# Performance work log

Hardware: AMD Instinct MI355X
Metric: run time of the kernel (lower is better)

The kernel has to match this reference:

```python
import jax, jax.numpy as jnp
import numpy as np

HEADS = 4
DIM_HEAD = 32


def setup_inputs() -> dict:
    key = jax.random.key(0)
    k0, k1, k2, k3 = jax.random.split(key, 4)
    b, C, H, W = 32, 128, 64, 64
    hidden = HEADS * DIM_HEAD
    x = jax.random.normal(k0, (b, C, H, W), dtype=jnp.float32)
    g = jnp.ones((C,), dtype=jnp.float32)                      # RMSNorm gain
    w_qkv = jax.random.normal(k1, (3 * hidden, C), dtype=jnp.float32) * 0.05
    mem_kv = jax.random.normal(k2, (2, HEADS, DIM_HEAD, 4), dtype=jnp.float32)
    w_out = jax.random.normal(k3, (C, hidden), dtype=jnp.float32) * 0.05
    b_out = jnp.zeros((C,), dtype=jnp.float32)
    return {"x": x, "g": g, "w_qkv": w_qkv, "mem_kv": mem_kv,
            "w_out": w_out, "b_out": b_out}


def reference(x, g, w_qkv, mem_kv, w_out, b_out):
    b, C, H, W = x.shape
    heads = mem_kv.shape[1]
    dh = mem_kv.shape[2]
    hidden = heads * dh
    scale = dh ** -0.5

    # RMSNorm variant: F.normalize along channel dim * g * sqrt(C)
    norm = jnp.maximum(jnp.sqrt(jnp.sum(x * x, axis=1, keepdims=True)), 1e-12)
    xn = x / norm * g[None, :, None, None] * (C ** 0.5)

    # 1x1 conv qkv projection (no bias)
    qkv = jnp.einsum('bchw,oc->bohw', xn, w_qkv)  # [b, 3*hidden, H, W]
    q, k, v = jnp.split(qkv, 3, axis=1)
    n = H * W
    q = q.reshape(b, heads, dh, n)
    k = k.reshape(b, heads, dh, n)
    v = v.reshape(b, heads, dh, n)

    # prepend memory kv slots along the token dim
    mk = jnp.broadcast_to(mem_kv[0][None], (b, heads, dh, mem_kv.shape[3]))
    mv = jnp.broadcast_to(mem_kv[1][None], (b, heads, dh, mem_kv.shape[3]))
    k = jnp.concatenate([mk, k], axis=-1)
    v = jnp.concatenate([mv, v], axis=-1)

    q = jax.nn.softmax(q, axis=-2) * scale   # softmax over feature dim d
    k = jax.nn.softmax(k, axis=-1)           # softmax over token dim n

    context = jnp.einsum('bhdn,bhen->bhde', k, v)   # [b,h,d,e]
    out = jnp.einsum('bhde,bhdn->bhen', context, q)  # [b,h,e,n]
    out = out.reshape(b, hidden, H, W)

    # 1x1 conv output projection (with bias)
    return jnp.einsum('bchw,oc->bohw', out, w_out) + b_out[None, :, None, None]
```

## Files before the change

kernel.cpp:

```cpp
#include <hip/hip_runtime.h>
#include <hip/hip_bf16.h>

typedef __attribute__((ext_vector_type(8))) short short8;
typedef __attribute__((ext_vector_type(4))) float f32x4;


__device__ __forceinline__ unsigned short f2bf(float f) {
  unsigned u = __float_as_uint(f);
  u += 0x7fff + ((u >> 16) & 1);
  return (unsigned short)(u >> 16);
}

__global__ void k0_init(const float* __restrict__ wqkv, const float* __restrict__ g,
                        float* __restrict__ ws) {
  int tid = blockIdx.x * blockDim.x + threadIdx.x;
  int stride = gridDim.x * blockDim.x;
  unsigned short* Wf = (unsigned short*)(ws + 2424832);
  for (int i = tid; i < 49152; i += stride) {
    int o = i >> 7, c = i & 127;
    int f = (o >> 4) * 4 + (c >> 5);
    int lane = (o & 15) + (((c >> 3) & 3) << 4);
    Wf[f * 512 + lane * 8 + (c & 7)] = f2bf(wqkv[o * 128 + c]);
  }
  float* gs = ws + 2449408;
  if (tid < 128) gs[tid] = g[tid] * 11.313708498984761f;
}

__global__ __launch_bounds__(256) void k1_qkv(
    const float* __restrict__ x, const unsigned short* __restrict__ Wf,
    const float* __restrict__ gs, float* __restrict__ Sp, float* __restrict__ Zp,
    unsigned short* __restrict__ qbf) {
  __shared__ __align__(16) unsigned short xnf[16 * 512];
  __shared__ unsigned short kbuf[128 * 66];
  __shared__ unsigned short vbuf[128 * 66];
  __shared__ float ssred[256];
  const int b = blockIdx.x >> 4, grp = blockIdx.x & 15;
  const int tid = threadIdx.x;
  const int p = tid & 63, w = tid >> 6;
  const int chunk = __builtin_amdgcn_readfirstlane(w);
  const int l = p, quad = l >> 4, l16 = l & 15;

  const int h4 = chunk, d0 = l16, eq = quad;
  float sacc0[8] = {}, sacc1[8] = {};
  float z0 = 0.f, z1 = 0.f;

  for (int t = 0; t < 4; t++) {
    const int tile = grp * 4 + t;
    const int P = tile * 64 + p;
    const float* xb = x + (size_t)b * 524288 + P;
    float xr[32];
    float ss = 0.f;
#pragma unroll
    for (int i = 0; i < 32; i++) {
      float v = xb[(size_t)(w * 32 + i) * 4096];
      xr[i] = v; ss += v * v;
    }
    ssred[w * 64 + p] = ss;
    __syncthreads();
    float tot = ssred[p] + ssred[64 + p] + ssred[128 + p] + ssred[192 + p];
    float inv = 1.0f / fmaxf(sqrtf(tot), 1e-12f);
#pragma unroll
    for (int q8 = 0; q8 < 4; q8++) {
      short8 v8;
#pragma unroll
      for (int j = 0; j < 8; j++) {
        int i = q8 * 8 + j;
        v8[j] = (short)f2bf(xr[i] * gs[w * 32 + i] * inv);
      }
      *(short8*)&xnf[(w * 4 + (p >> 4)) * 512 + ((p & 15) + q8 * 16) * 8] = v8;
    }
    __syncthreads();

    f32x4 acc[6][4] = {};
    const short8* Wfv = (const short8*)Wf;
#pragma unroll
    for (int k0 = 0; k0 < 4; k0++) {
      short8 bfr[4];
#pragma unroll
      for (int n0 = 0; n0 < 4; n0++)
        bfr[n0] = *(const short8*)&xnf[(k0 * 4 + n0) * 512 + l * 8];
#pragma unroll
      for (int m0 = 0; m0 < 6; m0++) {
        short8 afr = Wfv[((chunk * 6 + m0) * 4 + k0) * 64 + l];
#pragma unroll
        for (int n0 = 0; n0 < 4; n0++)
          acc[m0][n0] = __builtin_amdgcn_mfma_f32_16x16x32_bf16(afr, bfr[n0], acc[m0][n0], 0, 0, 0);
      }
    }
    __syncthreads();

#pragma unroll
    for (int s = 0; s < 3; s++) {
      int o0 = chunk * 96 + 32 * s;
      if (o0 < 128) {
        int h = o0 >> 5;
#pragma unroll
        for (int n0 = 0; n0 < 4; n0++) {
          float m = -1e30f;
#pragma unroll
          for (int off = 0; off < 2; off++)
#pragma unroll
            for (int r = 0; r < 4; r++) m = fmaxf(m, acc[2 * s + off][n0][r]);
          m = fmaxf(m, __shfl_xor(m, 16, 64));
          m = fmaxf(m, __shfl_xor(m, 32, 64));
          float e[2][4]; float sum = 0.f;
#pragma unroll
          for (int off = 0; off < 2; off++)
#pragma unroll
            for (int r = 0; r < 4; r++) {
              e[off][r] = __expf(acc[2 * s + off][n0][r] - m);
              sum += e[off][r];
            }
          sum += __shfl_xor(sum, 16, 64);
          sum += __shfl_xor(sum, 32, 64);
          float rs = 0.17677669529663687f / sum;
          int qbase = (h * 4 + n0) * 512;
#pragma unroll
          for (int off = 0; off < 2; off++)
#pragma unroll
            for (int r = 0; r < 4; r++) {
              int lane2 = l16 + ((off * 2 + (quad >> 1)) << 4);
              int jj = (quad & 1) * 4 + r;
              xnf[qbase + lane2 * 8 + jj] = f2bf(e[off][r] * rs);
            }
        }
      } else if (o0 < 256) {
        int r0 = o0 - 128;
#pragma unroll
        for (int n0 = 0; n0 < 4; n0++)
#pragma unroll
          for (int off = 0; off < 2; off++)
#pragma unroll
            for (int r = 0; r < 4; r++) {
              int row = r0 + off * 16 + quad * 4 + r;
              kbuf[row * 66 + n0 * 16 + l16] = f2bf(__expf(acc[2 * s + off][n0][r]));
            }
      } else {
        int r0 = o0 - 256;
#pragma unroll
        for (int n0 = 0; n0 < 4; n0++)
#pragma unroll
          for (int off = 0; off < 2; off++)
#pragma unroll
            for (int r = 0; r < 4; r++) {
              int row = r0 + off * 16 + quad * 4 + r;
              vbuf[row * 66 + n0 * 16 + l16] = f2bf(acc[2 * s + off][n0][r]);
            }
      }
    }
    __syncthreads();

    {
      const short8* qs = (const short8*)xnf;
      short8* qg = ((short8*)qbf) + (size_t)(b * 64 + tile) * 16 * 64;
#pragma unroll
      for (int r = 0; r < 4; r++) qg[tid + 256 * r] = qs[tid + 256 * r];
    }
    const unsigned short* kr0 = kbuf + (h4 * 32 + d0) * 66;
    const unsigned short* kr1 = kr0 + 16 * 66;
    const unsigned short* vr = vbuf + (h4 * 32 + 8 * eq) * 66;
#pragma unroll 4
    for (int pp = 0; pp < 32; pp++) {
      unsigned ka = *(const unsigned*)&kr0[2 * pp];
      unsigned kc = *(const unsigned*)&kr1[2 * pp];
      float k0e = __uint_as_float(ka << 16), k0o = __uint_as_float(ka & 0xffff0000u);
      float k1e = __uint_as_float(kc << 16), k1o = __uint_as_float(kc & 0xffff0000u);
      z0 += k0e + k0o; z1 += k1e + k1o;
#pragma unroll
      for (int j = 0; j < 8; j++) {
        unsigned vv = *(const unsigned*)&vr[j * 66 + 2 * pp];
        float ve = __uint_as_float(vv << 16), vo = __uint_as_float(vv & 0xffff0000u);
        sacc0[j] += k0e * ve + k0o * vo;
        sacc1[j] += k1e * ve + k1o * vo;
      }
    }
  }

  float* Spb = Sp + (size_t)(b * 16 + grp) * 4096;
  f32x4 s0a = {sacc0[0], sacc0[1], sacc0[2], sacc0[3]};
  f32x4 s0b = {sacc0[4], sacc0[5], sacc0[6], sacc0[7]};
  f32x4 s1a = {sacc1[0], sacc1[1], sacc1[2], sacc1[3]};
  f32x4 s1b = {sacc1[4], sacc1[5], sacc1[6], sacc1[7]};
  *(f32x4*)&Spb[(h4 * 32 + d0) * 32 + 8 * eq] = s0a;
  *(f32x4*)&Spb[(h4 * 32 + d0) * 32 + 8 * eq + 4] = s0b;
  *(f32x4*)&Spb[(h4 * 32 + d0 + 16) * 32 + 8 * eq] = s1a;
  *(f32x4*)&Spb[(h4 * 32 + d0 + 16) * 32 + 8 * eq + 4] = s1b;
  if (eq == 0) {
    Zp[(b * 16 + grp) * 128 + h4 * 32 + d0] = z0;
    Zp[(b * 16 + grp) * 128 + h4 * 32 + d0 + 16] = z1;
  }
}

__global__ void k2_ctx(const float* __restrict__ Sp, const float* __restrict__ Zp,
                       const float* __restrict__ memkv, const float* __restrict__ wout,
                       unsigned short* __restrict__ Mtf) {
  __shared__ float C[1024];
  __shared__ float zinv[128];
  const int b = blockIdx.x >> 2, qr = blockIdx.x & 3, tid = threadIdx.x;
  if (tid < 128) {
    float z = 0.f;
#pragma unroll
    for (int g = 0; g < 16; g++) z += Zp[(b * 16 + g) * 128 + tid];
    float zm = 0.f;
#pragma unroll
    for (int j = 0; j < 4; j++) zm += __expf(memkv[tid * 4 + j]);
    zinv[tid] = 1.0f / (z + zm);
  }
  __syncthreads();
  for (int i = tid; i < 1024; i += 256) {
    int idx = qr * 1024 + i;
    int hd = idx >> 5, e = idx & 31, h = hd >> 5;
    float s = 0.f;
#pragma unroll
    for (int g = 0; g < 16; g++) s += Sp[(size_t)(b * 16 + g) * 4096 + idx];
    float sm = 0.f;
#pragma unroll
    for (int j = 0; j < 4; j++)
      sm += __expf(memkv[hd * 4 + j]) * memkv[512 + (h * 32 + e) * 4 + j];
    C[i] = (s + sm) * zinv[hd];
  }
  __syncthreads();
  for (int i = tid; i < 4096; i += 256) {
    int hd = qr * 32 + (i >> 7);
    int o = i & 127, h = hd >> 5;
    float a = 0.f;
#pragma unroll
    for (int e = 0; e < 32; e++) a += wout[o * 128 + h * 32 + e] * C[(i >> 7) * 32 + e];
    int f = (o >> 4) * 4 + (hd >> 5);
    int lane = (o & 15) + (((hd >> 3) & 3) << 4);
    Mtf[(size_t)b * 16384 + f * 512 + lane * 8 + (hd & 7)] = f2bf(a);
  }
}

__global__ __launch_bounds__(256) void k3_out(
    const unsigned short* __restrict__ qbf, const unsigned short* __restrict__ Mtf,
    const float* __restrict__ bout, float* __restrict__ out) {
  __shared__ __align__(16) unsigned short qf[16 * 512];
  const int b = blockIdx.x >> 6, tile = blockIdx.x & 63;
  const int tid = threadIdx.x;
  const int l = tid & 63, quad = l >> 4, l16 = l & 15;
  const int chunk = __builtin_amdgcn_readfirstlane(tid >> 6);
  const short8* qv = (const short8*)qbf;
  const int base = ((b * 64 + tile) * 16) * 64;
#pragma unroll
  for (int r = 0; r < 4; r++) {
    int cid = tid + 256 * r;
    *(short8*)&qf[cid * 8] = qv[base + cid];
  }
  __syncthreads();
  f32x4 acc[2][4] = {};
  const short8* Mv = (const short8*)Mtf;
#pragma unroll
  for (int k0 = 0; k0 < 4; k0++) {
    short8 bfr[4];
#pragma unroll
    for (int n0 = 0; n0 < 4; n0++)
      bfr[n0] = *(const short8*)&qf[(k0 * 4 + n0) * 512 + l * 8];
#pragma unroll
    for (int mm = 0; mm < 2; mm++) {
      short8 afr = Mv[((size_t)b * 32 + (chunk * 2 + mm) * 4 + k0) * 64 + l];
#pragma unroll
      for (int n0 = 0; n0 < 4; n0++)
        acc[mm][n0] = __builtin_amdgcn_mfma_f32_16x16x32_bf16(afr, bfr[n0], acc[mm][n0], 0, 0, 0);
    }
  }
  float bv[2][4];
#pragma unroll
  for (int mm = 0; mm < 2; mm++)
#pragma unroll
    for (int r = 0; r < 4; r++) bv[mm][r] = bout[chunk * 32 + mm * 16 + quad * 4 + r];
#pragma unroll
  for (int mm = 0; mm < 2; mm++)
#pragma unroll
    for (int n0 = 0; n0 < 4; n0++)
#pragma unroll
      for (int r = 0; r < 4; r++) {
        int o = chunk * 32 + mm * 16 + quad * 4 + r;
        int Pp = tile * 64 + n0 * 16 + l16;
        out[((size_t)b * 128 + o) * 4096 + Pp] = acc[mm][n0][r] + bv[mm][r];
      }
}

extern "C" void kernel_launch(void* const* d_in, const int* in_sizes, int n_in,
                              void* d_out, int out_size, void* d_ws, size_t ws_size,
                              hipStream_t stream) {
  const float* x     = (const float*)d_in[0];
  const float* g     = (const float*)d_in[1];
  const float* wqkv  = (const float*)d_in[2];
  const float* memkv = (const float*)d_in[3];
  const float* wout  = (const float*)d_in[4];
  const float* bout  = (const float*)d_in[5];
  float* out = (float*)d_out;
  float* ws = (float*)d_ws;
  float* Sp  = ws;
  float* Zp  = ws + 2097152;
  unsigned short* Mtf = (unsigned short*)(ws + 2162688);
  unsigned short* Wf  = (unsigned short*)(ws + 2424832);
  float* gs  = ws + 2449408;
  unsigned short* qbf = (unsigned short*)(ws + 2449536);

  k0_init<<<128, 256, 0, stream>>>(wqkv, g, ws);
  k1_qkv<<<512, 256, 0, stream>>>(x, Wf, gs, Sp, Zp, qbf);
  k2_ctx<<<128, 256, 0, stream>>>(Sp, Zp, memkv, wout, Mtf);
  k3_out<<<2048, 256, 0, stream>>>(qbf, Mtf, bout, out);
}
```

Before: 232.2 us.

## Split qkv projection into per-slice MFMA passes, double grid, bf16 partials, coalesced output

The qkv kernel now computes its MFMA accumulators one 32-row slice at a time rather than holding all six, which cuts register pressure, and it adds launch bounds targeting four blocks per SIMD. The grid is doubled to 1024 blocks, each handling 2 tiles. Softmaxed q is written straight to global memory with no staging copy through shared memory. Per-block context and normalizer partials are stored as bf16, halving their traffic, at some cost in accuracy when the 32 partials are summed. The output kernel stages results in shared memory so global stores are 16-byte coalesced rows, at the cost of extra LDS and a barrier.

```diff
diff --git a/kernel.cpp b/kernel.cpp
--- a/kernel.cpp
+++ b/kernel.cpp
@@ -9,6 +9,9 @@
   unsigned u = __float_as_uint(f);
   u += 0x7fff + ((u >> 16) & 1);
   return (unsigned short)(u >> 16);
+}
+__device__ __forceinline__ float bf2f(unsigned short s) {
+  return __uint_as_float(((unsigned)s) << 16);
 }
 
 __global__ void k0_init(const float* __restrict__ wqkv, const float* __restrict__ g,
@@ -26,15 +29,15 @@
   if (tid < 128) gs[tid] = g[tid] * 11.313708498984761f;
 }
 
-__global__ __launch_bounds__(256) void k1_qkv(
+__global__ __launch_bounds__(256, 4) void k1_qkv(
     const float* __restrict__ x, const unsigned short* __restrict__ Wf,
-    const float* __restrict__ gs, float* __restrict__ Sp, float* __restrict__ Zp,
-    unsigned short* __restrict__ qbf) {
+    const float* __restrict__ gs, unsigned short* __restrict__ Sp,
+    unsigned short* __restrict__ Zp, unsigned short* __restrict__ qbf) {
   __shared__ __align__(16) unsigned short xnf[16 * 512];
   __shared__ unsigned short kbuf[128 * 66];
   __shared__ unsigned short vbuf[128 * 66];
   __shared__ float ssred[256];
-  const int b = blockIdx.x >> 4, grp = blockIdx.x & 15;
+  const int b = blockIdx.x >> 5, grp = blockIdx.x & 31;
   const int tid = threadIdx.x;
   const int p = tid & 63, w = tid >> 6;
   const int chunk = __builtin_amdgcn_readfirstlane(w);
@@ -44,8 +47,8 @@
   float sacc0[8] = {}, sacc1[8] = {};
   float z0 = 0.f, z1 = 0.f;
 
-  for (int t = 0; t < 4; t++) {
-    const int tile = grp * 4 + t;
+  for (int t = 0; t < 2; t++) {
+    const int tile = grp * 2 + t;
     const int P = tile * 64 + p;
     const float* xb = x + (size_t)b * 524288 + P;
     float xr[32];
@@ -71,27 +74,25 @@
     }
     __syncthreads();
 
-    f32x4 acc[6][4] = {};
     const short8* Wfv = (const short8*)Wf;
 #pragma unroll
-    for (int k0 = 0; k0 < 4; k0++) {
-      short8 bfr[4];
-#pragma unroll
-      for (int n0 = 0; n0 < 4; n0++)
-        bfr[n0] = *(const short8*)&xnf[(k0 * 4 + n0) * 512 + l * 8];
-#pragma unroll
-      for (int m0 = 0; m0 < 6; m0++) {
-        short8 afr = Wfv[((chunk * 6 + m0) * 4 + k0) * 64 + l];
+    for (int s = 0; s < 3; s++) {
+      f32x4 acc[2][4] = {};
+#pragma unroll
+      for (int k0 = 0; k0 < 4; k0++) {
+        short8 bfr[4];
 #pragma unroll
         for (int n0 = 0; n0 < 4; n0++)
-          acc[m0][n0] = __builtin_amdgcn_mfma_f32_16x16x32_bf16(afr, bfr[n0], acc[m0][n0], 0, 0, 0);
-      }
-    }
-    __syncthreads();
-
-#pragma unroll
-    for (int s = 0; s < 3; s++) {
-      int o0 = chunk * 96 + 32 * s;
+          bfr[n0] = *(const short8*)&xnf[(k0 * 4 + n0) * 512 + l * 8];
+#pragma unroll
+        for (int off = 0; off < 2; off++) {
+          short8 afr = Wfv[((chunk * 6 + 2 * s + off) * 4 + k0) * 64 + l];
+#pragma unroll
+          for (int n0 = 0; n0 < 4; n0++)
+            acc[off][n0] = __builtin_amdgcn_mfma_f32_16x16x32_bf16(afr, bfr[n0], acc[off][n0], 0, 0, 0);
+        }
+      }
+      const int o0 = chunk * 96 + 32 * s;
       if (o0 < 128) {
         int h = o0 >> 5;
 #pragma unroll
@@ -100,7 +101,7 @@
 #pragma unroll
           for (int off = 0; off < 2; off++)
 #pragma unroll
-            for (int r = 0; r < 4; r++) m = fmaxf(m, acc[2 * s + off][n0][r]);
+            for (int r = 0; r < 4; r++) m = fmaxf(m, acc[off][n0][r]);
           m = fmaxf(m, __shfl_xor(m, 16, 64));
           m = fmaxf(m, __shfl_xor(m, 32, 64));
           float e[2][4]; float sum = 0.f;
@@ -108,54 +109,48 @@
           for (int off = 0; off < 2; off++)
 #pragma unroll
             for (int r = 0; r < 4; r++) {
-              e[off][r] = __expf(acc[2 * s + off][n0][r] - m);
+              e[off][r] = __expf(acc[off][n0][r] - m);
               sum += e[off][r];
             }
           sum += __shfl_xor(sum, 16, 64);
           sum += __shfl_xor(sum, 32, 64);
           float rs = 0.17677669529663687f / sum;
-          int qbase = (h * 4 + n0) * 512;
+          int qbase = ((b * 64 + tile) * 16 + h * 4 + n0) * 512;
 #pragma unroll
           for (int off = 0; off < 2; off++)
 #pragma unroll
             for (int r = 0; r < 4; r++) {
               int lane2 = l16 + ((off * 2 + (quad >> 1)) << 4);
               int jj = (quad & 1) * 4 + r;
-              xnf[qbase + lane2 * 8 + jj] = f2bf(e[off][r] * rs);
+              qbf[qbase + lane2 * 8 + jj] = f2bf(e[off][r] * rs);
             }
         }
       } else if (o0 < 256) {
-        int r0 = o0 - 128;
+        int h = (o0 - 128) >> 5;
 #pragma unroll
         for (int n0 = 0; n0 < 4; n0++)
 #pragma unroll
           for (int off = 0; off < 2; off++)
 #pragma unroll
             for (int r = 0; r < 4; r++) {
-              int row = r0 + off * 16 + quad * 4 + r;
-              kbuf[row * 66 + n0 * 16 + l16] = f2bf(__expf(acc[2 * s + off][n0][r]));
+              int row = h * 32 + off * 16 + quad * 4 + r;
+              kbuf[row * 66 + n0 * 16 + l16] = f2bf(__expf(acc[off][n0][r]));
             }
       } else {
-        int r0 = o0 - 256;
+        int h = (o0 - 256) >> 5;
 #pragma unroll
         for (int n0 = 0; n0 < 4; n0++)
 #pragma unroll
           for (int off = 0; off < 2; off++)
 #pragma unroll
             for (int r = 0; r < 4; r++) {
-              int row = r0 + off * 16 + quad * 4 + r;
-              vbuf[row * 66 + n0 * 16 + l16] = f2bf(acc[2 * s + off][n0][r]);
+              int row = h * 32 + off * 16 + quad * 4 + r;
+              vbuf[row * 66 + n0 * 16 + l16] = f2bf(acc[off][n0][r]);
             }
       }
     }
     __syncthreads();
 
-    {
-      const short8* qs = (const short8*)xnf;
-      short8* qg = ((short8*)qbf) + (size_t)(b * 64 + tile) * 16 * 64;
-#pragma unroll
-      for (int r = 0; r < 4; r++) qg[tid + 256 * r] = qs[tid + 256 * r];
-    }
     const unsigned short* kr0 = kbuf + (h4 * 32 + d0) * 66;
     const unsigned short* kr1 = kr0 + 16 * 66;
     const unsigned short* vr = vbuf + (h4 * 32 + 8 * eq) * 66;
@@ -176,22 +171,19 @@
     }
   }
 
-  float* Spb = Sp + (size_t)(b * 16 + grp) * 4096;
-  f32x4 s0a = {sacc0[0], sacc0[1], sacc0[2], sacc0[3]};
-  f32x4 s0b = {sacc0[4], sacc0[5], sacc0[6], sacc0[7]};
-  f32x4 s1a = {sacc1[0], sacc1[1], sacc1[2], sacc1[3]};
-  f32x4 s1b = {sacc1[4], sacc1[5], sacc1[6], sacc1[7]};
-  *(f32x4*)&Spb[(h4 * 32 + d0) * 32 + 8 * eq] = s0a;
-  *(f32x4*)&Spb[(h4 * 32 + d0) * 32 + 8 * eq + 4] = s0b;
-  *(f32x4*)&Spb[(h4 * 32 + d0 + 16) * 32 + 8 * eq] = s1a;
-  *(f32x4*)&Spb[(h4 * 32 + d0 + 16) * 32 + 8 * eq + 4] = s1b;
+  unsigned short* Spb = Sp + (size_t)(b * 32 + grp) * 4096;
+  short8 s0, s1;
+#pragma unroll
+  for (int j = 0; j < 8; j++) { s0[j] = (short)f2bf(sacc0[j]); s1[j] = (short)f2bf(sacc1[j]); }
+  *(short8*)&Spb[(h4 * 32 + d0) * 32 + 8 * eq] = s0;
+  *(short8*)&Spb[(h4 * 32 + d0 + 16) * 32 + 8 * eq] = s1;
   if (eq == 0) {
-    Zp[(b * 16 + grp) * 128 + h4 * 32 + d0] = z0;
-    Zp[(b * 16 + grp) * 128 + h4 * 32 + d0 + 16] = z1;
-  }
-}
-
-__global__ void k2_ctx(const float* __restrict__ Sp, const float* __restrict__ Zp,
+    Zp[(b * 32 + grp) * 128 + h4 * 32 + d0] = f2bf(z0);
+    Zp[(b * 32 + grp) * 128 + h4 * 32 + d0 + 16] = f2bf(z1);
+  }
+}
+
+__global__ void k2_ctx(const unsigned short* __restrict__ Sp, const unsigned short* __restrict__ Zp,
                        const float* __restrict__ memkv, const float* __restrict__ wout,
                        unsigned short* __restrict__ Mtf) {
   __shared__ float C[1024];
@@ -200,7 +192,7 @@
   if (tid < 128) {
     float z = 0.f;
 #pragma unroll
-    for (int g = 0; g < 16; g++) z += Zp[(b * 16 + g) * 128 + tid];
+    for (int g = 0; g < 32; g++) z += bf2f(Zp[(b * 32 + g) * 128 + tid]);
     float zm = 0.f;
 #pragma unroll
     for (int j = 0; j < 4; j++) zm += __expf(memkv[tid * 4 + j]);
@@ -212,7 +204,7 @@
     int hd = idx >> 5, e = idx & 31, h = hd >> 5;
     float s = 0.f;
 #pragma unroll
-    for (int g = 0; g < 16; g++) s += Sp[(size_t)(b * 16 + g) * 4096 + idx];
+    for (int g = 0; g < 32; g++) s += bf2f(Sp[(size_t)(b * 32 + g) * 4096 + idx]);
     float sm = 0.f;
 #pragma unroll
     for (int j = 0; j < 4; j++)
@@ -236,6 +228,7 @@
     const unsigned short* __restrict__ qbf, const unsigned short* __restrict__ Mtf,
     const float* __restrict__ bout, float* __restrict__ out) {
   __shared__ __align__(16) unsigned short qf[16 * 512];
+  __shared__ __align__(16) float obuf[128 * 68];
   const int b = blockIdx.x >> 6, tile = blockIdx.x & 63;
   const int tid = threadIdx.x;
   const int l = tid & 63, quad = l >> 4, l16 = l & 15;
@@ -264,21 +257,25 @@
         acc[mm][n0] = __builtin_amdgcn_mfma_f32_16x16x32_bf16(afr, bfr[n0], acc[mm][n0], 0, 0, 0);
     }
   }
-  float bv[2][4];
 #pragma unroll
   for (int mm = 0; mm < 2; mm++)
 #pragma unroll
-    for (int r = 0; r < 4; r++) bv[mm][r] = bout[chunk * 32 + mm * 16 + quad * 4 + r];
-#pragma unroll
-  for (int mm = 0; mm < 2; mm++)
-#pragma unroll
-    for (int n0 = 0; n0 < 4; n0++)
-#pragma unroll
-      for (int r = 0; r < 4; r++) {
+    for (int r = 0; r < 4; r++) {
+      float bv = bout[chunk * 32 + mm * 16 + quad * 4 + r];
+#pragma unroll
+      for (int n0 = 0; n0 < 4; n0++) {
         int o = chunk * 32 + mm * 16 + quad * 4 + r;
-        int Pp = tile * 64 + n0 * 16 + l16;
-        out[((size_t)b * 128 + o) * 4096 + Pp] = acc[mm][n0][r] + bv[mm][r];
-      }
+        obuf[o * 68 + n0 * 16 + l16] = acc[mm][n0][r] + bv;
+      }
+    }
+  __syncthreads();
+#pragma unroll
+  for (int rr = 0; rr < 8; rr++) {
+    int idx = tid + 256 * rr;
+    int row = idx >> 4, c4 = idx & 15;
+    f32x4 v = *(const f32x4*)&obuf[row * 68 + c4 * 4];
+    *(f32x4*)&out[((size_t)b * 128 + row) * 4096 + tile * 64 + c4 * 4] = v;
+  }
 }
 
 extern "C" void kernel_launch(void* const* d_in, const int* in_sizes, int n_in,
@@ -292,15 +289,15 @@
   const float* bout  = (const float*)d_in[5];
   float* out = (float*)d_out;
   float* ws = (float*)d_ws;
-  float* Sp  = ws;
-  float* Zp  = ws + 2097152;
+  unsigned short* Sp  = (unsigned short*)ws;
+  unsigned short* Zp  = (unsigned short*)(ws + 2097152);
   unsigned short* Mtf = (unsigned short*)(ws + 2162688);
   unsigned short* Wf  = (unsigned short*)(ws + 2424832);
   float* gs  = ws + 2449408;
   unsigned short* qbf = (unsigned short*)(ws + 2449536);
 
   k0_init<<<128, 256, 0, stream>>>(wqkv, g, ws);
-  k1_qkv<<<512, 256, 0, stream>>>(x, Wf, gs, Sp, Zp, qbf);
+  k1_qkv<<<1024, 256, 0, stream>>>(x, Wf, gs, Sp, Zp, qbf);
   k2_ctx<<<128, 256, 0, stream>>>(Sp, Zp, memkv, wout, Mtf);
   k3_out<<<2048, 256, 0, stream>>>(qbf, Mtf, bout, out);
 }
```

New measurement: 196.7 us. -15.3%, faster.
